# Performance work log

Hardware: AMD Instinct MI355X
Metric: run time of the kernel (lower is better)

The kernel has to match this reference:

```python
import jax, jax.numpy as jnp
import numpy as np

S, B, T = 2048, 256, 64


def setup_inputs() -> dict:
    key = jax.random.key(0)
    k_em, k_tag, k_st, k_et, k_tr = jax.random.split(key, 5)
    emissions = jax.random.normal(k_em, (S, B, T), dtype=jnp.float32)
    tags = jax.random.randint(k_tag, (S, B), 0, T)
    mask = jnp.ones((S, B), dtype=bool)
    start_transitions = jax.random.uniform(k_st, (T,), minval=-0.1, maxval=0.1, dtype=jnp.float32)
    end_transitions = jax.random.uniform(k_et, (T,), minval=-0.1, maxval=0.1, dtype=jnp.float32)
    transitions = jax.random.uniform(k_tr, (T, T), minval=-0.1, maxval=0.1, dtype=jnp.float32)
    return {
        "emissions": emissions,
        "tags": tags,
        "mask": mask,
        "start_transitions": start_transitions,
        "end_transitions": end_transitions,
        "transitions": transitions,
    }


def _crf_llh(emissions, tags, mask, start_transitions, end_transitions, transitions):
    # emissions: [S, B, T]; tags/mask: [S, B]
    seq_len, batch, _ = emissions.shape
    maskf = mask.astype(emissions.dtype)
    barange = jnp.arange(batch)

    # ---- numerator: score of the gold tag sequence ----
    em_tag = jnp.take_along_axis(emissions, tags[:, :, None], axis=2)[:, :, 0]  # [S, B]
    trans_tag = transitions[tags[:-1], tags[1:]]  # [S-1, B]
    numerator = (
        start_transitions[tags[0]]
        + em_tag[0]
        + jnp.sum((trans_tag + em_tag[1:]) * maskf[1:], axis=0)
    )
    seq_ends = mask.astype(jnp.int32).sum(axis=0) - 1  # [B]
    last_tags = tags[seq_ends, barange]
    numerator = numerator + end_transitions[last_tags]

    # ---- denominator: log partition via forward-algorithm scan ----
    def step(score, xs):
        em_i, m_i = xs  # [B, T], [B]
        # [B, T_prev, 1] + [T_prev, T_next] + [B, 1, T_next] -> logsumexp over T_prev
        nxt = jax.nn.logsumexp(score[:, :, None] + transitions[None, :, :] + em_i[:, None, :], axis=1)
        return jnp.where(m_i[:, None], nxt, score), None

    score0 = start_transitions + emissions[0]  # [B, T]
    score, _ = jax.lax.scan(step, score0, (emissions[1:], mask[1:]))
    denominator = jax.nn.logsumexp(score + end_transitions, axis=1)  # [B]

    llh = numerator - denominator
    return llh.sum()  # reduction='sum'


def reference(emissions, tags, mask, start_transitions, end_transitions, transitions):
    return _crf_llh(emissions, tags, mask, start_transitions, end_transitions, transitions)
```

## Files before the change

### kernel.cpp

```cpp
#include <hip/hip_runtime.h>
#include <stdint.h>


#define S_LEN 2048
#define B_SZ  256
#define T_SZ  64
#define BT    (B_SZ * T_SZ)

__global__ __launch_bounds__(128, 1) void crf_fused(
    const float* __restrict__ em, const int* __restrict__ tags,
    const float* __restrict__ startt, const float* __restrict__ endt,
    const float* __restrict__ trans, float* __restrict__ llh_out)
{
    const int b    = blockIdx.x;
    const int tid  = threadIdx.x;
    const int wid  = tid >> 6;
    const int lane = tid & 63;

    __shared__ float s_num;
    __shared__ __align__(16) float p_lds[T_SZ];
    __shared__ __align__(16) float et[T_SZ * T_SZ];

    for (int idx = tid; idx < T_SZ * T_SZ; idx += 128) {
        const int i    = idx >> 6;
        const int jj   = idx & 63;
        const int slot = (i >> 2) ^ (jj & 15);
        et[jj * T_SZ + slot * 4 + (i & 3)] = __expf(trans[idx]);
    }
    __syncthreads();

    if (wid == 1) {
        float part = 0.f;
        for (int s = lane; s < S_LEN; s += 64) {
            const int tg = tags[s * B_SZ + b];
            if (s == 0) {
                part += startt[tg] + em[(size_t)b * T_SZ + tg];
            } else {
                const int tgp = tags[(s - 1) * B_SZ + b];
                part += trans[tgp * T_SZ + tg] + em[((size_t)s * B_SZ + b) * T_SZ + tg];
            }
        }
        #pragma unroll
        for (int d = 32; d >= 1; d >>= 1) part += __shfl_down(part, d, 64);
        if (lane == 0) {
            const int lastt = tags[(S_LEN - 1) * B_SZ + b];
            s_num = part + endt[lastt];
        }
        __syncthreads();
        return;
    }

    const int j  = lane;
    const int jx = j & 15;
    const float* etrow = &et[j * T_SZ];

    float score = startt[j] + em[(size_t)b * T_SZ + j];

    const float* ep = em + ((size_t)B_SZ + b) * T_SZ + j;
    float e0 = ep[0];
    float e1 = ep[BT];
    float e2 = ep[2 * BT];
    float e3 = ep[3 * BT];

    #pragma unroll 4
    for (int s = 1; s < S_LEN; ++s) {
        const float epf = (s + 4 < S_LEN) ? ep[4 * BT] : 0.0f;

        const float m = __int_as_float(__builtin_amdgcn_readfirstlane(__float_as_int(score)));
        const float p = __expf(score - m);

        p_lds[j] = p;

        float a0 = 0.f, a1 = 0.f, a2 = 0.f, a3 = 0.f;
        #pragma unroll
        for (int g = 0; g < 16; ++g) {
            const float4 pg = *reinterpret_cast<const float4*>(&p_lds[g * 4]);
            const float4 eg = *reinterpret_cast<const float4*>(&etrow[(g ^ jx) * 4]);
            a0 = fmaf(pg.x, eg.x, a0);
            a1 = fmaf(pg.y, eg.y, a1);
            a2 = fmaf(pg.z, eg.z, a2);
            a3 = fmaf(pg.w, eg.w, a3);
        }
        score = e0 + m + __logf((a0 + a1) + (a2 + a3));

        e0 = e1; e1 = e2; e2 = e3; e3 = epf;
        ep += BT;
    }

    float v = score + endt[j];
    float mx = v;
    #pragma unroll
    for (int d = 1; d < 64; d <<= 1) mx = fmaxf(mx, __shfl_xor(mx, d, 64));
    float e = __expf(v - mx);
    #pragma unroll
    for (int d = 1; d < 64; d <<= 1) e += __shfl_xor(e, d, 64);

    __syncthreads();
    if (j == 0) {
        const float denom = mx + __logf(e);
        llh_out[b] = s_num - denom;
    }
}

__global__ __launch_bounds__(64, 1) void crf_reduce(
    const float* __restrict__ llh, float* __restrict__ out)
{
    const int lane = threadIdx.x;
    double acc = 0.0;
    #pragma unroll
    for (int i = 0; i < B_SZ / 64; ++i) acc += (double)llh[i * 64 + lane];
    #pragma unroll
    for (int d = 32; d >= 1; d >>= 1) acc += __shfl_down(acc, d, 64);
    if (lane == 0) out[0] = (float)acc;
}

extern "C" void kernel_launch(void* const* d_in, const int* in_sizes, int n_in,
                              void* d_out, int out_size, void* d_ws, size_t ws_size,
                              hipStream_t stream)
{
    const float* em     = (const float*)d_in[0];
    const int*   tags   = (const int*)d_in[1];
    const float* startt = (const float*)d_in[3];
    const float* endt   = (const float*)d_in[4];
    const float* trans  = (const float*)d_in[5];
    float* out    = (float*)d_out;
    float* llh_ws = (float*)d_ws;

    crf_fused <<<B_SZ, 128, 0, stream>>>(em, tags, startt, endt, trans, llh_ws);
    crf_reduce<<<1,    64,  0, stream>>>(llh_ws, out);
}
```

Before: 852.1 us.

## Split CRF forward recurrence across four waves in linear-probability space

The per-step matrix-vector product is spread over four scan waves: each handles 16 target tags, and within a wave four lane groups each take a quarter of the source tags, combined with cross-lane shuffles. The recurrence now carries probabilities instead of log scores, with power-of-two renormalisation every 8 steps. This removes the per-step exp/log and shortens each step's serial dot product. In exchange every step needs a block-wide barrier (the numerator wave joins each one too), and underflow or overflow can occur between renormalisations.

Result: faster. 770.5 us (-9.6%).

```diff
diff --git a/kernel.cpp b/kernel.cpp
--- a/kernel.cpp
+++ b/kernel.cpp
@@ -1,104 +1,143 @@
 #include <hip/hip_runtime.h>
 #include <stdint.h>
+#include <math.h>
 
 
 #define S_LEN 2048
 #define B_SZ  256
 #define T_SZ  64
 #define BT    (B_SZ * T_SZ)
+#define NW_SCAN 4
+#define NTHREADS (NW_SCAN * 64 + 64)
+#define RENORM 8
 
-__global__ __launch_bounds__(128, 1) void crf_fused(
+__device__ __forceinline__ void wave_barrier() {
+    asm volatile("s_waitcnt lgkmcnt(0)\n\ts_barrier" ::: "memory");
+    __builtin_amdgcn_sched_barrier(0);
+}
+
+__global__ __launch_bounds__(NTHREADS, 1) void crf_fused(
     const float* __restrict__ em, const int* __restrict__ tags,
     const float* __restrict__ startt, const float* __restrict__ endt,
     const float* __restrict__ trans, float* __restrict__ llh_out)
 {
-    const int b    = blockIdx.x;
-    const int tid  = threadIdx.x;
-    const int wid  = tid >> 6;
-    const int lane = tid & 63;
+    const int b   = blockIdx.x;
+    const int tid = threadIdx.x;
+    const int wv  = tid >> 6;
+    const int l   = tid & 63;
 
     __shared__ float s_num;
-    __shared__ __align__(16) float p_lds[T_SZ];
+    __shared__ __align__(16) float w_lds[2][T_SZ];
+    __shared__ __align__(16) float sc_lds[T_SZ];
     __shared__ __align__(16) float et[T_SZ * T_SZ];
 
-    for (int idx = tid; idx < T_SZ * T_SZ; idx += 128) {
+    for (int idx = tid; idx < T_SZ * T_SZ; idx += NTHREADS) {
         const int i    = idx >> 6;
         const int jj   = idx & 63;
         const int slot = (i >> 2) ^ (jj & 15);
         et[jj * T_SZ + slot * 4 + (i & 3)] = __expf(trans[idx]);
     }
+    if (tid < T_SZ) {
+        w_lds[0][tid] = __expf(startt[tid] + em[(size_t)b * T_SZ + tid]);
+    }
     __syncthreads();
 
-    if (wid == 1) {
+    if (wv == NW_SCAN) {
         float part = 0.f;
-        for (int s = lane; s < S_LEN; s += 64) {
-            const int tg = tags[s * B_SZ + b];
-            if (s == 0) {
-                part += startt[tg] + em[(size_t)b * T_SZ + tg];
-            } else {
-                const int tgp = tags[(s - 1) * B_SZ + b];
-                part += trans[tgp * T_SZ + tg] + em[((size_t)s * B_SZ + b) * T_SZ + tg];
+        for (int k = 0; k < S_LEN - 1; ++k) {
+            if ((k & 63) == 0 && (k >> 6) < 32) {
+                const int s  = (k >> 6) * 64 + l;
+                const int tg = tags[s * B_SZ + b];
+                if (s == 0) {
+                    part += startt[tg] + em[(size_t)b * T_SZ + tg];
+                } else {
+                    const int tgp = tags[(s - 1) * B_SZ + b];
+                    part += trans[tgp * T_SZ + tg] + em[((size_t)s * B_SZ + b) * T_SZ + tg];
+                }
             }
+            if (k == 2040) {
+                #pragma unroll
+                for (int d = 32; d >= 1; d >>= 1) part += __shfl_down(part, d, 64);
+                if (l == 0) {
+                    const int lastt = tags[(S_LEN - 1) * B_SZ + b];
+                    s_num = part + endt[lastt];
+                }
+            }
+            wave_barrier();
         }
-        #pragma unroll
-        for (int d = 32; d >= 1; d >>= 1) part += __shfl_down(part, d, 64);
-        if (lane == 0) {
-            const int lastt = tags[(S_LEN - 1) * B_SZ + b];
-            s_num = part + endt[lastt];
-        }
-        __syncthreads();
+        wave_barrier();
         return;
     }
 
-    const int j  = lane;
-    const int jx = j & 15;
-    const float* etrow = &et[j * T_SZ];
+    const int q  = l >> 4;
+    const int jj = (wv << 4) + (l & 15);
+    const int jx = jj & 15;
+    const float* etbase = &et[jj * T_SZ];
+    const bool leader = (q == 0);
 
-    float score = startt[j] + em[(size_t)b * T_SZ + j];
+    const float* ep = em + ((size_t)B_SZ + b) * T_SZ + jj;
+    float r0 = ep[0];
+    float r1 = ep[BT];
+    float r2 = ep[2 * BT];
+    float r3 = ep[3 * BT];
 
-    const float* ep = em + ((size_t)B_SZ + b) * T_SZ + j;
-    float e0 = ep[0];
-    float e1 = ep[BT];
-    float e2 = ep[2 * BT];
-    float e3 = ep[3 * BT];
+    float L   = 0.f;
+    float wme = 0.f;
+    int   cur = 0;
 
     #pragma unroll 4
     for (int s = 1; s < S_LEN; ++s) {
-        const float epf = (s + 4 < S_LEN) ? ep[4 * BT] : 0.0f;
-
-        const float m = __int_as_float(__builtin_amdgcn_readfirstlane(__float_as_int(score)));
-        const float p = __expf(score - m);
-
-        p_lds[j] = p;
+        const float rpf = (s + 4 < S_LEN) ? ep[4 * BT] : 0.0f;
 
         float a0 = 0.f, a1 = 0.f, a2 = 0.f, a3 = 0.f;
         #pragma unroll
-        for (int g = 0; g < 16; ++g) {
-            const float4 pg = *reinterpret_cast<const float4*>(&p_lds[g * 4]);
-            const float4 eg = *reinterpret_cast<const float4*>(&etrow[(g ^ jx) * 4]);
-            a0 = fmaf(pg.x, eg.x, a0);
-            a1 = fmaf(pg.y, eg.y, a1);
-            a2 = fmaf(pg.z, eg.z, a2);
-            a3 = fmaf(pg.w, eg.w, a3);
+        for (int t = 0; t < 4; ++t) {
+            const float4 wg = *reinterpret_cast<const float4*>(&w_lds[cur][q * 16 + t * 4]);
+            const float4 eg = *reinterpret_cast<const float4*>(&etbase[((4 * q + t) ^ jx) * 4]);
+            a0 = fmaf(wg.x, eg.x, a0);
+            a1 = fmaf(wg.y, eg.y, a1);
+            a2 = fmaf(wg.z, eg.z, a2);
+            a3 = fmaf(wg.w, eg.w, a3);
         }
-        score = e0 + m + __logf((a0 + a1) + (a2 + a3));
+        float v = (a0 + a1) + (a2 + a3);
+        v += __shfl_xor(v, 16, 64);
+        v += __shfl_xor(v, 32, 64);
 
-        e0 = e1; e1 = e2; e2 = e3; e3 = epf;
+        float wnew = v * __expf(r0);
+
+        if ((s & (RENORM - 1)) == 0) {
+            const float w0 = w_lds[cur][0];
+            int ex;
+            (void)frexpf(w0, &ex);
+            const float rs = __int_as_float((127 - ex) << 23);
+            wnew *= rs;
+            L += (float)ex * 0.6931471805599453f;
+        }
+
+        if (leader) w_lds[cur ^ 1][jj] = wnew;
+        wme = wnew;
+
+        r0 = r1; r1 = r2; r2 = r3; r3 = rpf;
         ep += BT;
+        cur ^= 1;
+        wave_barrier();
     }
 
-    float v = score + endt[j];
-    float mx = v;
-    #pragma unroll
-    for (int d = 1; d < 64; d <<= 1) mx = fmaxf(mx, __shfl_xor(mx, d, 64));
-    float e = __expf(v - mx);
-    #pragma unroll
-    for (int d = 1; d < 64; d <<= 1) e += __shfl_xor(e, d, 64);
+    if (leader) sc_lds[jj] = __logf(wme) + L + endt[jj];
+    wave_barrier();
 
-    __syncthreads();
-    if (j == 0) {
-        const float denom = mx + __logf(e);
-        llh_out[b] = s_num - denom;
+    if (wv == 0) {
+        const float sv = sc_lds[l];
+        float mx = sv;
+        #pragma unroll
+        for (int d = 1; d < 64; d <<= 1) mx = fmaxf(mx, __shfl_xor(mx, d, 64));
+        float e = __expf(sv - mx);
+        #pragma unroll
+        for (int d = 1; d < 64; d <<= 1) e += __shfl_xor(e, d, 64);
+        if (l == 0) {
+            const float denom = mx + __logf(e);
+            llh_out[b] = s_num - denom;
+        }
     }
 }
 
@@ -126,6 +165,6 @@
     float* out    = (float*)d_out;
     float* llh_ws = (float*)d_ws;
 
-    crf_fused <<<B_SZ, 128, 0, stream>>>(em, tags, startt, endt, trans, llh_ws);
-    crf_reduce<<<1,    64,  0, stream>>>(llh_ws, out);
+    crf_fused <<<B_SZ, NTHREADS, 0, stream>>>(em, tags, startt, endt, trans, llh_ws);
+    crf_reduce<<<1,    64,       0, stream>>>(llh_ws, out);
 }
```
